# Kernel optimization log

Hardware: AMD Instinct MI355X
Metric: run time of the kernel (lower is better)

The kernel has to match this reference:

```python
import jax, jax.numpy as jnp
import numpy as np

B, R, L, K = 64, 196, 512, 768
NEG = jnp.float32(-2**31 + 1)


def setup_inputs() -> dict:
    key = jax.random.key(0)
    ks = jax.random.split(key, 8)
    image_emb = jax.random.normal(ks[0], (B, R, L), dtype=jnp.float32)
    seq_emb = jax.random.normal(ks[1], (B, L, K), dtype=jnp.float32)
    mask = jax.random.randint(ks[2], (B, L), 0, 2, dtype=jnp.int32)
    # Linear(l,1) and Linear(k,1) params, Xavier-ish scale
    image_W = jax.random.normal(ks[3], (L, 1), dtype=jnp.float32) / np.sqrt(L)
    image_b = jnp.zeros((1,), dtype=jnp.float32)
    seq_W = jax.random.normal(ks[4], (K, 1), dtype=jnp.float32) / np.sqrt(K)
    seq_b = jnp.zeros((1,), dtype=jnp.float32)
    # V_weight [L, L], xavier_uniform
    lim = np.sqrt(6.0 / (L + L)).astype(np.float32)
    V_weight = jax.random.uniform(ks[5], (L, L), dtype=jnp.float32, minval=-lim, maxval=lim)
    return {"image_emb": image_emb, "seq_emb": seq_emb, "mask": mask,
            "image_W": image_W, "image_b": image_b,
            "seq_W": seq_W, "seq_b": seq_b, "V_weight": V_weight}


def reference(image_emb, seq_emb, mask, image_W, image_b, seq_W, seq_b, V_weight):
    # p: [B,R,1], q: [B,L,1]
    p = jnp.tanh(image_emb @ image_W + image_b)
    q = jnp.tanh(seq_emb @ seq_W + seq_b)
    qt = jnp.swapaxes(q, 1, 2)              # [B,1,L]
    emb = p @ qt + qt                       # [B,R,L] (rank-1 outer + broadcast add)
    score = emb @ V_weight                  # [B,R,L]
    # dropout_rate=0.0 -> identity
    score = jnp.where(mask[:, None, :] == 0, NEG, score)
    score = jax.nn.softmax(score, axis=-1)  # [B,R,L]
    out = score @ seq_emb                   # [B,R,K]
    out = out / jnp.sqrt(jnp.float32(seq_emb.shape[-1]))
    return out
```

## Files before the change

kernel.cpp:

```cpp
#include <hip/hip_runtime.h>
#include <cstdint>
#include <cstddef>


typedef __attribute__((ext_vector_type(8))) short short8;
typedef __attribute__((ext_vector_type(4))) float f32x4;

__device__ __forceinline__ unsigned short f32_to_bf16(float x) {
    unsigned int u = __float_as_uint(x);
    unsigned int r = (u + 0x7FFFu + ((u >> 16) & 1u)) >> 16;
    return (unsigned short)r;
}
__device__ __forceinline__ float bf16_to_f32(unsigned short h) {
    return __uint_as_float(((unsigned int)h) << 16);
}

#if defined(__has_builtin)
#if __has_builtin(__builtin_amdgcn_cvt_pk_bf16_f32)
#define HAVE_PK_BF16 1
#endif
#endif

__device__ __forceinline__ unsigned int pk_bf16(float a, float b) {
#ifdef HAVE_PK_BF16
    typedef __attribute__((ext_vector_type(2))) __bf16 bf16x2;
    bf16x2 v = __builtin_amdgcn_cvt_pk_bf16_f32(a, b);
    return __builtin_bit_cast(unsigned int, v);
#else
    return (unsigned int)f32_to_bf16(a) | ((unsigned int)f32_to_bf16(b) << 16);
#endif
}

__global__ __launch_bounds__(256) void kprep(const float* __restrict__ seq,
                                             const float* __restrict__ seqW,
                                             const float* __restrict__ img,
                                             const float* __restrict__ imgW,
                                             const float* __restrict__ imgBias,
                                             unsigned short* __restrict__ seqT,
                                             float* __restrict__ qpart,
                                             float* __restrict__ pv) {
    __shared__ __align__(16) unsigned int sT[128 * 32];
    __shared__ __align__(16) float sWc[128];

    if (blockIdx.x >= 3072) {
        int wv = threadIdx.x >> 6, lane = threadIdx.x & 63;
        int row = (blockIdx.x - 3072) * 4 + wv;
        const float4* x4 = (const float4*)(img + (size_t)row * 512);
        const float4* w4 = (const float4*)imgW;
        float s = 0.f;
#pragma unroll
        for (int i = 0; i < 2; ++i) {
            float4 a = x4[i * 64 + lane];
            float4 c = w4[i * 64 + lane];
            s += a.x * c.x + a.y * c.y + a.z * c.z + a.w * c.w;
        }
#pragma unroll
        for (int o = 32; o; o >>= 1) s += __shfl_xor(s, o, 64);
        if (lane == 0) pv[row] = tanhf(s + imgBias[0]);
        return;
    }

    int id = blockIdx.x;
    int b = id / 48, rem = id - b * 48;
    int jt = rem / 6, ck = rem - jt * 6;
    int j0 = jt * 64;
    int t = threadIdx.x;
    if (t < 128) sWc[t] = seqW[ck * 128 + t];

    int quad = t >> 4, kseg = t & 15;
    int qk = quad ^ kseg;
    const float* base = seq + (size_t)b * 512 * 768 + (size_t)(j0 + quad * 4) * 768 + ck * 128;
    int jg = t & 7, krow = t >> 3;
    float qp[4] = {0.f, 0.f, 0.f, 0.f};
    __syncthreads();

#pragma unroll
    for (int rp = 0; rp < 2; ++rp) {
        int kq = rp * 64 + kseg * 4;
        float4 r0 = *(const float4*)(base + 0 * 768 + kq);
        float4 r1 = *(const float4*)(base + 1 * 768 + kq);
        float4 r2 = *(const float4*)(base + 2 * 768 + kq);
        float4 r3 = *(const float4*)(base + 3 * 768 + kq);
        float4 w  = *(const float4*)(sWc + kq);
        qp[0] += r0.x * w.x + r0.y * w.y + r0.z * w.z + r0.w * w.w;
        qp[1] += r1.x * w.x + r1.y * w.y + r1.z * w.z + r1.w * w.w;
        qp[2] += r2.x * w.x + r2.y * w.y + r2.z * w.z + r2.w * w.w;
        qp[3] += r3.x * w.x + r3.y * w.y + r3.z * w.z + r3.w * w.w;
        float a0[4] = {r0.x, r0.y, r0.z, r0.w};
        float a1[4] = {r1.x, r1.y, r1.z, r1.w};
        float a2[4] = {r2.x, r2.y, r2.z, r2.w};
        float a3[4] = {r3.x, r3.y, r3.z, r3.w};
#pragma unroll
        for (int i = 0; i < 4; ++i) {
            int k = kq + i;
            int col = (qk ^ (i << 2)) & 15;
            uint2 v;
            v.x = pk_bf16(a0[i], a1[i]);
            v.y = pk_bf16(a2[i], a3[i]);
            *(uint2*)(sT + k * 32 + col * 2) = v;
        }
    }
    __syncthreads();
    unsigned short* dst = seqT + (((size_t)b * 6 + ck) * 8 + jt) * (128 * 64);
#pragma unroll
    for (int wp = 0; wp < 4; ++wp) {
        int k = wp * 32 + krow;
        int s = ((k >> 2) & 15) ^ ((k & 3) << 2);
        int sw = (k ^ (k >> 3)) & 7;
        int jgOut = jg ^ sw;
        int c0 = ((jgOut << 1) ^ s) & 15;
        int c1 = c0 ^ 1;
        uint2 va = *(const uint2*)(sT + k * 32 + c0 * 2);
        uint2 vb = *(const uint2*)(sT + k * 32 + c1 * 2);
        uint4 o;
        o.x = va.x; o.y = va.y; o.z = vb.x; o.w = vb.y;
        *(uint4*)(dst + (size_t)k * 64 + jg * 8) = o;
    }
#pragma unroll
    for (int rr = 0; rr < 4; ++rr) {
        float s = qp[rr];
        s += __shfl_xor(s, 8, 64);
        s += __shfl_xor(s, 4, 64);
        s += __shfl_xor(s, 2, 64);
        s += __shfl_xor(s, 1, 64);
        if (kseg == 0)
            qpart[(size_t)ck * 32768 + b * 512 + j0 + quad * 4 + rr] = s;
    }
}

__global__ __launch_bounds__(256) void krows_p(const float* __restrict__ x,
                                               const float* __restrict__ w,
                                               const float* __restrict__ bias,
                                               float* __restrict__ outp) {
    int wv = threadIdx.x >> 6, lane = threadIdx.x & 63;
    int row = blockIdx.x * 4 + wv;
    const float4* x4 = (const float4*)(x + (size_t)row * 512);
    const float4* w4 = (const float4*)w;
    float s = 0.f;
#pragma unroll
    for (int i = 0; i < 2; ++i) {
        float4 a = x4[i * 64 + lane];
        float4 c = w4[i * 64 + lane];
        s += a.x * c.x + a.y * c.y + a.z * c.z + a.w * c.w;
    }
#pragma unroll
    for (int o = 32; o; o >>= 1) s += __shfl_xor(s, o, 64);
    if (lane == 0) outp[row] = tanhf(s + bias[0]);
}

__global__ __launch_bounds__(256) void krows_q(const float* __restrict__ x,
                                               const float* __restrict__ w,
                                               float* __restrict__ outp) {
    int wv = threadIdx.x >> 6, lane = threadIdx.x & 63;
    int row = blockIdx.x * 4 + wv;
    const float4* x4 = (const float4*)(x + (size_t)row * 768);
    const float4* w4 = (const float4*)w;
    float s = 0.f;
#pragma unroll
    for (int i = 0; i < 3; ++i) {
        float4 a = x4[i * 64 + lane];
        float4 c = w4[i * 64 + lane];
        s += a.x * c.x + a.y * c.y + a.z * c.z + a.w * c.w;
    }
#pragma unroll
    for (int o = 32; o; o >>= 1) s += __shfl_xor(s, o, 64);
    if (lane == 0) outp[row] = s;
}

__global__ __launch_bounds__(256) void kw(const float* __restrict__ qpart,
                                          const float* __restrict__ seqBias,
                                          const float* __restrict__ V,
                                          const int* __restrict__ mask,
                                          float* __restrict__ wm,
                                          int nparts) {
    __shared__ __align__(16) float sq[512];
    __shared__ __align__(16) float sacc[16][16][4];
    int b = blockIdx.x >> 3, jc = blockIdx.x & 7;
    int t = threadIdx.x;
    float qb = seqBias[0];
    float a0 = 0.f, a1 = 0.f;
    for (int pp = 0; pp < nparts; ++pp) {
        a0 += qpart[(size_t)pp * 32768 + b * 512 + t];
        a1 += qpart[(size_t)pp * 32768 + b * 512 + t + 256];
    }
    sq[t] = tanhf(a0 + qb);
    sq[t + 256] = tanhf(a1 + qb);
    __syncthreads();
    int jt = t & 15, lg = t >> 4;
    const float4* V4 = (const float4*)V;
    int col4 = jc * 16 + jt;
    float ax = 0.f, ay = 0.f, az = 0.f, aw = 0.f;
    int lbase = lg * 32;
#pragma unroll 8
    for (int li = 0; li < 32; ++li) {
        int l = lbase + li;
        float qq = sq[l];
        float4 v = V4[(size_t)l * 128 + col4];
        ax += qq * v.x; ay += qq * v.y; az += qq * v.z; aw += qq * v.w;
    }
    sacc[lg][jt][0] = ax; sacc[lg][jt][1] = ay;
    sacc[lg][jt][2] = az; sacc[lg][jt][3] = aw;
    __syncthreads();
    if (t < 16) {
        float sx = 0.f, sy = 0.f, sz = 0.f, sw = 0.f;
#pragma unroll
        for (int g = 0; g < 16; ++g) {
            sx += sacc[g][t][0]; sy += sacc[g][t][1];
            sz += sacc[g][t][2]; sw += sacc[g][t][3];
        }
        const int* mrow = mask + b * 512 + jc * 64 + t * 4;
        float4 o;
        o.x = mrow[0] ? sx : -1e30f;
        o.y = mrow[1] ? sy : -1e30f;
        o.z = mrow[2] ? sz : -1e30f;
        o.w = mrow[3] ? sw : -1e30f;
        ((float4*)(wm + b * 512 + jc * 64))[t] = o;
    }
}

__global__ __launch_bounds__(256, 2) void kattn2(const unsigned short* __restrict__ seqT,
                                                 const float* __restrict__ p,
                                                 const float* __restrict__ wm,
                                                 float* __restrict__ out) {
    __shared__ __align__(16) unsigned short sB[2][128 * 64];
    __shared__ __align__(16) float swm[512];
    __shared__ float sinvz[64];
    __shared__ float sred[16];

    int raw = blockIdx.x;
    int g  = ((raw >> 5) << 3) + (raw & 7);
    int rt = (raw >> 3) & 3;
    int b  = g / 6, nt = g - b * 6;
    int t  = threadIdx.x;
    int wv = t >> 6, lane = t & 63;
    int mm = lane & 15, q = lane >> 4;
    int nb = nt * 128;

    float v0 = wm[b * 512 + t];
    float v1 = wm[b * 512 + t + 256];
    swm[t] = v0; swm[t + 256] = v1;
    float lmax = fmaxf(v0, v1);
    float fa = (v0 > -1e29f) ? v0 : 1e30f;
    float fb = (v1 > -1e29f) ? v1 : 1e30f;
    float lmin = fminf(fa, fb);
#pragma unroll
    for (int o = 32; o; o >>= 1) {
        lmax = fmaxf(lmax, __shfl_xor(lmax, o, 64));
        lmin = fminf(lmin, __shfl_xor(lmin, o, 64));
    }
    if (lane == 0) { sred[wv] = lmax; sred[8 + wv] = lmin; }
    __syncthreads();

    bool wactive = (rt * 64 + wv * 16) < 196;

    int rl = wv * 16 + mm;
    int r  = rt * 64 + rl;
    bool valid = r < 196;

    short8 afrag[16];
    if (wactive) {
        float wmax = fmaxf(fmaxf(sred[0], sred[1]), fmaxf(sred[2], sred[3]));
        float wmin = fminf(fminf(sred[8], sred[9]), fminf(sred[10], sred[11]));
        int pidx = b * 196 + (valid ? r : 195);
        float c = 1.0f + p[pidx];
        float M = (c >= 0.f) ? c * wmax : c * wmin;

        float zsum = 0.f;
        const f32x4* swm4 = (const f32x4*)swm;
#pragma unroll
        for (int tk = 0; tk < 16; ++tk) {
            int jb = tk * 32 + q * 8;
            f32x4 w0 = swm4[jb >> 2];
            f32x4 w1 = swm4[(jb >> 2) + 1];
            short8 af;
#pragma unroll
            for (int jj = 0; jj < 8; ++jj) {
                float ww = (jj < 4) ? w0[jj] : w1[jj - 4];
                float e = valid ? __expf(c * ww - M) : 0.f;
                unsigned short h = f32_to_bf16(e);
                zsum += bf16_to_f32(h);
                af[jj] = (short)h;
            }
            afrag[tk] = af;
        }
        zsum += __shfl_xor(zsum, 16, 64);
        zsum += __shfl_xor(zsum, 32, 64);
        if (q == 0) sinvz[rl] = 1.0f / zsum;
    }

    f32x4 acc[8];
#pragma unroll
    for (int s = 0; s < 8; ++s) acc[s] = (f32x4){0.f, 0.f, 0.f, 0.f};

    const unsigned short* seqTb = seqT + ((size_t)(b * 6 + nt) * 8) * (128 * 64);
    int toff = t * 8;
    auto stage = [&](int ch, int buf) {
        const unsigned short* src = seqTb + (size_t)ch * 8192 + toff;
        unsigned short* ld = sB[buf] + toff;
        short8 v0 = *(const short8*)(src);
        short8 v1 = *(const short8*)(src + 2048);
        short8 v2 = *(const short8*)(src + 4096);
        short8 v3 = *(const short8*)(src + 6144);
        *(short8*)(ld)        = v0;
        *(short8*)(ld + 2048) = v1;
        *(short8*)(ld + 4096) = v2;
        *(short8*)(ld + 6144) = v3;
    };

    __syncthreads();
    stage(0, 0);
    __syncthreads();
#pragma unroll
    for (int ch = 0; ch < 8; ++ch) {
        if (ch < 7) stage(ch + 1, (ch + 1) & 1);
        if (wactive) {
            const unsigned short* cb = sB[ch & 1];
#pragma unroll
            for (int kk = 0; kk < 2; ++kk) {
                short8 bfr[8];
#pragma unroll
                for (int s = 0; s < 8; ++s) {
                    int n = s * 16 + mm;
                    int sw = (n ^ (n >> 3)) & 7;
                    bfr[s] = *(const short8*)(cb + n * 64 + ((((kk << 2) + q) ^ sw) << 3));
                }
#pragma unroll
                for (int s = 0; s < 8; ++s)
                    acc[s] = __builtin_amdgcn_mfma_f32_16x16x32_bf16(
                        afrag[(ch << 1) + kk], bfr[s], acc[s], 0, 0, 0);
            }
        }
        __syncthreads();
    }

    if (wactive) {
        const float invsqrtk = 0.036084391824351615f;
#pragma unroll
        for (int reg = 0; reg < 4; ++reg) {
            int row = q * 4 + reg;
            int rr = rt * 64 + wv * 16 + row;
            if (rr < 196) {
                float scale = sinvz[wv * 16 + row] * invsqrtk;
                float* op = out + (size_t)(b * 196 + rr) * 768 + nb + mm;
#pragma unroll
                for (int s = 0; s < 8; ++s)
                    op[s * 16] = acc[s][reg] * scale;
            }
        }
    }
}

__global__ __launch_bounds__(256, 2) void kattn(const float* __restrict__ seq,
                                                const float* __restrict__ p,
                                                const float* __restrict__ wm,
                                                float* __restrict__ out) {
    __shared__ __align__(16) unsigned int sseq[2][128 * 32];
    __shared__ __align__(16) float swm[512];
    __shared__ float sinvz[64];
    __shared__ float sred[16];

    int id = blockIdx.x;
    int rt = id & 3;
    int nt = (id >> 2) % 6;
    int b  = id / 24;
    int t  = threadIdx.x;
    int wv = t >> 6, lane = t & 63;
    int mm = lane & 15, q = lane >> 4;
    int nb = nt * 128;

    float v0 = wm[b * 512 + t];
    float v1 = wm[b * 512 + t + 256];
    swm[t] = v0; swm[t + 256] = v1;
    float lmax = fmaxf(v0, v1);
    float fa = (v0 > -1e29f) ? v0 : 1e30f;
    float fb = (v1 > -1e29f) ? v1 : 1e30f;
    float lmin = fminf(fa, fb);
#pragma unroll
    for (int o = 32; o; o >>= 1) {
        lmax = fmaxf(lmax, __shfl_xor(lmax, o, 64));
        lmin = fminf(lmin, __shfl_xor(lmin, o, 64));
    }
    if (lane == 0) { sred[wv] = lmax; sred[8 + wv] = lmin; }
    __syncthreads();
    float wmax = fmaxf(fmaxf(sred[0], sred[1]), fmaxf(sred[2], sred[3]));
    float wmin = fminf(fminf(sred[8], sred[9]), fminf(sred[10], sred[11]));

    int rl = wv * 16 + mm;
    int r  = rt * 64 + rl;
    bool valid = r < 196;
    int pidx = b * 196 + (valid ? r : 195);
    float c = 1.0f + p[pidx];
    float M = (c >= 0.f) ? c * wmax : c * wmin;

    short8 afrag[16];
    float zsum = 0.f;
    const f32x4* swm4 = (const f32x4*)swm;
#pragma unroll
    for (int tk = 0; tk < 16; ++tk) {
        int jb = tk * 32 + q * 8;
        f32x4 w0 = swm4[jb >> 2];
        f32x4 w1 = swm4[(jb >> 2) + 1];
        short8 af;
#pragma unroll
        for (int jj = 0; jj < 8; ++jj) {
            float ww = (jj < 4) ? w0[jj] : w1[jj - 4];
            float e = valid ? __expf(c * ww - M) : 0.f;
            unsigned short h = f32_to_bf16(e);
            zsum += bf16_to_f32(h);
            af[jj] = (short)h;
        }
        afrag[tk] = af;
    }
    zsum += __shfl_xor(zsum, 16, 64);
    zsum += __shfl_xor(zsum, 32, 64);
    if (q == 0) sinvz[rl] = 1.0f / zsum;

    f32x4 acc[8];
#pragma unroll
    for (int s = 0; s < 8; ++s) acc[s] = (f32x4){0.f, 0.f, 0.f, 0.f};

    const float* seqb = seq + (size_t)b * 512 * 768 + nb;
    int tl = t & 31, jp = t >> 5;
    int n0 = tl * 4;
    auto stage = [&](int ch, int buf) {
        unsigned int* sb = sseq[buf];
#pragma unroll
        for (int pass = 0; pass < 4; ++pass) {
            int jl = pass * 16 + jp * 2;
            int jglob = ch * 64 + jl;
            float4 a0 = *(const float4*)(seqb + (size_t)jglob * 768 + n0);
            float4 a1 = *(const float4*)(seqb + (size_t)(jglob + 1) * 768 + n0);
            float a0v[4] = {a0.x, a0.y, a0.z, a0.w};
            float a1v[4] = {a1.x, a1.y, a1.z, a1.w};
            int g = jl >> 3;
            int wo = (jl & 7) >> 1;
#pragma unroll
            for (int i = 0; i < 4; ++i) {
                int n = n0 + i;
                int sw = (n ^ (n >> 3)) & 7;
                unsigned int pk = (unsigned int)f32_to_bf16(a0v[i]) |
                                  ((unsigned int)f32_to_bf16(a1v[i]) << 16);
                sb[n * 32 + ((g ^ sw) << 2) + wo] = pk;
            }
        }
    };

    __syncthreads();
    stage(0, 0);
    __syncthreads();
#pragma unroll
    for (int ch = 0; ch < 8; ++ch) {
        if (ch < 7) stage(ch + 1, (ch + 1) & 1);
        const unsigned int* cb = sseq[ch & 1];
#pragma unroll
        for (int kk = 0; kk < 2; ++kk) {
            short8 bfr[8];
#pragma unroll
            for (int s = 0; s < 8; ++s) {
                int n = s * 16 + mm;
                int g = kk * 4 + q;
                int sw = (n ^ (n >> 3)) & 7;
                bfr[s] = *(const short8*)(cb + n * 32 + ((g ^ sw) << 2));
            }
#pragma unroll
            for (int s = 0; s < 8; ++s)
                acc[s] = __builtin_amdgcn_mfma_f32_16x16x32_bf16(
                    afrag[ch * 2 + kk], bfr[s], acc[s], 0, 0, 0);
        }
        __syncthreads();
    }

    const float invsqrtk = 0.036084391824351615f;
#pragma unroll
    for (int reg = 0; reg < 4; ++reg) {
        int row = q * 4 + reg;
        int rr = rt * 64 + wv * 16 + row;
        if (rr < 196) {
            float scale = sinvz[wv * 16 + row] * invsqrtk;
            float* op = out + (size_t)(b * 196 + rr) * 768 + nb + mm;
#pragma unroll
            for (int s = 0; s < 8; ++s)
                op[s * 16] = acc[s][reg] * scale;
        }
    }
}

extern "C" void kernel_launch(void* const* d_in, const int* in_sizes, int n_in,
                              void* d_out, int out_size, void* d_ws, size_t ws_size,
                              hipStream_t stream) {
    const float* image_emb = (const float*)d_in[0];
    const float* seq_emb   = (const float*)d_in[1];
    const int*   mask      = (const int*)d_in[2];
    const float* image_W   = (const float*)d_in[3];
    const float* image_b   = (const float*)d_in[4];
    const float* seq_W     = (const float*)d_in[5];
    const float* seq_b     = (const float*)d_in[6];
    const float* V         = (const float*)d_in[7];
    float* out = (float*)d_out;

    float* p_ws  = (float*)d_ws;
    float* qpart = (float*)((char*)d_ws + (128 << 10));
    float* wm_ws = (float*)((char*)d_ws + (896 << 10));
    unsigned short* seqT = (unsigned short*)((char*)d_ws + (1024 << 10));

    size_t need = (size_t)(1024 << 10) + (size_t)64 * 768 * 512 * 2;
    if (ws_size >= need) {
        kprep<<<dim3(6208), dim3(256), 0, stream>>>(seq_emb, seq_W,
                                                    image_emb, image_W, image_b,
                                                    seqT, qpart, p_ws);
        kw<<<dim3(512), dim3(256), 0, stream>>>(qpart, seq_b, V, mask, wm_ws, 6);
        kattn2<<<dim3(1536), dim3(256), 0, stream>>>(seqT, p_ws, wm_ws, out);
    } else {
        krows_p<<<dim3(3136), dim3(256), 0, stream>>>(image_emb, image_W, image_b, p_ws);
        krows_q<<<dim3(8192), dim3(256), 0, stream>>>(seq_emb, seq_W, qpart);
        kw<<<dim3(512), dim3(256), 0, stream>>>(qpart, seq_b, V, mask, wm_ws, 1);
        kattn<<<dim3(1536), dim3(256), 0, stream>>>(seq_emb, p_ws, wm_ws, out);
    }
}
```

Measured before the change: 234.0 us.

## Drop bf16 transposed seq copy; stream fp32 seq directly with register-prefetch pipeline

Removes the prep pass that wrote a transposed bf16 copy of seq_emb to workspace. The attention kernel now reads fp32 seq_emb directly. Loads for the next chunk are issued into registers before the MFMA work and written to shared memory afterward, so global latency overlaps compute. Also merges the q and p row-dot kernels into one launch and skips inactive waves. This saves a full write and re-read of a 50MB intermediate, at the cost of reading fp32 (twice the bytes) inside attention and converting it per block across 6 column tiles.

New measurement: 252.7 us. +8.0%, slower.

```diff
diff --git a/kernel.cpp b/kernel.cpp
--- a/kernel.cpp
+++ b/kernel.cpp
@@ -31,20 +31,30 @@
 #endif
 }
 
-__global__ __launch_bounds__(256) void kprep(const float* __restrict__ seq,
-                                             const float* __restrict__ seqW,
-                                             const float* __restrict__ img,
-                                             const float* __restrict__ imgW,
-                                             const float* __restrict__ imgBias,
-                                             unsigned short* __restrict__ seqT,
-                                             float* __restrict__ qpart,
-                                             float* __restrict__ pv) {
-    __shared__ __align__(16) unsigned int sT[128 * 32];
-    __shared__ __align__(16) float sWc[128];
-
-    if (blockIdx.x >= 3072) {
-        int wv = threadIdx.x >> 6, lane = threadIdx.x & 63;
-        int row = (blockIdx.x - 3072) * 4 + wv;
+__global__ __launch_bounds__(256) void kqp(const float* __restrict__ seq,
+                                           const float* __restrict__ seqW,
+                                           const float* __restrict__ img,
+                                           const float* __restrict__ imgW,
+                                           const float* __restrict__ imgBias,
+                                           float* __restrict__ qraw,
+                                           float* __restrict__ pv) {
+    int wv = threadIdx.x >> 6, lane = threadIdx.x & 63;
+    if (blockIdx.x < 8192) {
+        int row = blockIdx.x * 4 + wv;
+        const float4* x4 = (const float4*)(seq + (size_t)row * 768);
+        const float4* w4 = (const float4*)seqW;
+        float s = 0.f;
+#pragma unroll
+        for (int i = 0; i < 3; ++i) {
+            float4 a = x4[i * 64 + lane];
+            float4 c = w4[i * 64 + lane];
+            s += a.x * c.x + a.y * c.y + a.z * c.z + a.w * c.w;
+        }
+#pragma unroll
+        for (int o = 32; o; o >>= 1) s += __shfl_xor(s, o, 64);
+        if (lane == 0) qraw[row] = s;
+    } else {
+        int row = (blockIdx.x - 8192) * 4 + wv;
         const float4* x4 = (const float4*)(img + (size_t)row * 512);
         const float4* w4 = (const float4*)imgW;
         float s = 0.f;
@@ -57,134 +67,21 @@
 #pragma unroll
         for (int o = 32; o; o >>= 1) s += __shfl_xor(s, o, 64);
         if (lane == 0) pv[row] = tanhf(s + imgBias[0]);
-        return;
-    }
-
-    int id = blockIdx.x;
-    int b = id / 48, rem = id - b * 48;
-    int jt = rem / 6, ck = rem - jt * 6;
-    int j0 = jt * 64;
-    int t = threadIdx.x;
-    if (t < 128) sWc[t] = seqW[ck * 128 + t];
-
-    int quad = t >> 4, kseg = t & 15;
-    int qk = quad ^ kseg;
-    const float* base = seq + (size_t)b * 512 * 768 + (size_t)(j0 + quad * 4) * 768 + ck * 128;
-    int jg = t & 7, krow = t >> 3;
-    float qp[4] = {0.f, 0.f, 0.f, 0.f};
-    __syncthreads();
-
-#pragma unroll
-    for (int rp = 0; rp < 2; ++rp) {
-        int kq = rp * 64 + kseg * 4;
-        float4 r0 = *(const float4*)(base + 0 * 768 + kq);
-        float4 r1 = *(const float4*)(base + 1 * 768 + kq);
-        float4 r2 = *(const float4*)(base + 2 * 768 + kq);
-        float4 r3 = *(const float4*)(base + 3 * 768 + kq);
-        float4 w  = *(const float4*)(sWc + kq);
-        qp[0] += r0.x * w.x + r0.y * w.y + r0.z * w.z + r0.w * w.w;
-        qp[1] += r1.x * w.x + r1.y * w.y + r1.z * w.z + r1.w * w.w;
-        qp[2] += r2.x * w.x + r2.y * w.y + r2.z * w.z + r2.w * w.w;
-        qp[3] += r3.x * w.x + r3.y * w.y + r3.z * w.z + r3.w * w.w;
-        float a0[4] = {r0.x, r0.y, r0.z, r0.w};
-        float a1[4] = {r1.x, r1.y, r1.z, r1.w};
-        float a2[4] = {r2.x, r2.y, r2.z, r2.w};
-        float a3[4] = {r3.x, r3.y, r3.z, r3.w};
-#pragma unroll
-        for (int i = 0; i < 4; ++i) {
-            int k = kq + i;
-            int col = (qk ^ (i << 2)) & 15;
-            uint2 v;
-            v.x = pk_bf16(a0[i], a1[i]);
-            v.y = pk_bf16(a2[i], a3[i]);
-            *(uint2*)(sT + k * 32 + col * 2) = v;
-        }
-    }
-    __syncthreads();
-    unsigned short* dst = seqT + (((size_t)b * 6 + ck) * 8 + jt) * (128 * 64);
-#pragma unroll
-    for (int wp = 0; wp < 4; ++wp) {
-        int k = wp * 32 + krow;
-        int s = ((k >> 2) & 15) ^ ((k & 3) << 2);
-        int sw = (k ^ (k >> 3)) & 7;
-        int jgOut = jg ^ sw;
-        int c0 = ((jgOut << 1) ^ s) & 15;
-        int c1 = c0 ^ 1;
-        uint2 va = *(const uint2*)(sT + k * 32 + c0 * 2);
-        uint2 vb = *(const uint2*)(sT + k * 32 + c1 * 2);
-        uint4 o;
-        o.x = va.x; o.y = va.y; o.z = vb.x; o.w = vb.y;
-        *(uint4*)(dst + (size_t)k * 64 + jg * 8) = o;
-    }
-#pragma unroll
-    for (int rr = 0; rr < 4; ++rr) {
-        float s = qp[rr];
-        s += __shfl_xor(s, 8, 64);
-        s += __shfl_xor(s, 4, 64);
-        s += __shfl_xor(s, 2, 64);
-        s += __shfl_xor(s, 1, 64);
-        if (kseg == 0)
-            qpart[(size_t)ck * 32768 + b * 512 + j0 + quad * 4 + rr] = s;
-    }
-}
-
-__global__ __launch_bounds__(256) void krows_p(const float* __restrict__ x,
-                                               const float* __restrict__ w,
-                                               const float* __restrict__ bias,
-                                               float* __restrict__ outp) {
-    int wv = threadIdx.x >> 6, lane = threadIdx.x & 63;
-    int row = blockIdx.x * 4 + wv;
-    const float4* x4 = (const float4*)(x + (size_t)row * 512);
-    const float4* w4 = (const float4*)w;
-    float s = 0.f;
-#pragma unroll
-    for (int i = 0; i < 2; ++i) {
-        float4 a = x4[i * 64 + lane];
-        float4 c = w4[i * 64 + lane];
-        s += a.x * c.x + a.y * c.y + a.z * c.z + a.w * c.w;
-    }
-#pragma unroll
-    for (int o = 32; o; o >>= 1) s += __shfl_xor(s, o, 64);
-    if (lane == 0) outp[row] = tanhf(s + bias[0]);
-}
-
-__global__ __launch_bounds__(256) void krows_q(const float* __restrict__ x,
-                                               const float* __restrict__ w,
-                                               float* __restrict__ outp) {
-    int wv = threadIdx.x >> 6, lane = threadIdx.x & 63;
-    int row = blockIdx.x * 4 + wv;
-    const float4* x4 = (const float4*)(x + (size_t)row * 768);
-    const float4* w4 = (const float4*)w;
-    float s = 0.f;
-#pragma unroll
-    for (int i = 0; i < 3; ++i) {
-        float4 a = x4[i * 64 + lane];
-        float4 c = w4[i * 64 + lane];
-        s += a.x * c.x + a.y * c.y + a.z * c.z + a.w * c.w;
-    }
-#pragma unroll
-    for (int o = 32; o; o >>= 1) s += __shfl_xor(s, o, 64);
-    if (lane == 0) outp[row] = s;
-}
-
-__global__ __launch_bounds__(256) void kw(const float* __restrict__ qpart,
+    }
+}
+
+__global__ __launch_bounds__(256) void kw(const float* __restrict__ qraw,
                                           const float* __restrict__ seqBias,
                                           const float* __restrict__ V,
                                           const int* __restrict__ mask,
-                                          float* __restrict__ wm,
-                                          int nparts) {
+                                          float* __restrict__ wm) {
     __shared__ __align__(16) float sq[512];
     __shared__ __align__(16) float sacc[16][16][4];
     int b = blockIdx.x >> 3, jc = blockIdx.x & 7;
     int t = threadIdx.x;
     float qb = seqBias[0];
-    float a0 = 0.f, a1 = 0.f;
-    for (int pp = 0; pp < nparts; ++pp) {
-        a0 += qpart[(size_t)pp * 32768 + b * 512 + t];
-        a1 += qpart[(size_t)pp * 32768 + b * 512 + t + 256];
-    }
-    sq[t] = tanhf(a0 + qb);
-    sq[t + 256] = tanhf(a1 + qb);
+    sq[t] = tanhf(qraw[b * 512 + t] + qb);
+    sq[t + 256] = tanhf(qraw[b * 512 + t + 256] + qb);
     __syncthreads();
     int jt = t & 15, lg = t >> 4;
     const float4* V4 = (const float4*)V;
@@ -218,138 +115,6 @@
     }
 }
 
-__global__ __launch_bounds__(256, 2) void kattn2(const unsigned short* __restrict__ seqT,
-                                                 const float* __restrict__ p,
-                                                 const float* __restrict__ wm,
-                                                 float* __restrict__ out) {
-    __shared__ __align__(16) unsigned short sB[2][128 * 64];
-    __shared__ __align__(16) float swm[512];
-    __shared__ float sinvz[64];
-    __shared__ float sred[16];
-
-    int raw = blockIdx.x;
-    int g  = ((raw >> 5) << 3) + (raw & 7);
-    int rt = (raw >> 3) & 3;
-    int b  = g / 6, nt = g - b * 6;
-    int t  = threadIdx.x;
-    int wv = t >> 6, lane = t & 63;
-    int mm = lane & 15, q = lane >> 4;
-    int nb = nt * 128;
-
-    float v0 = wm[b * 512 + t];
-    float v1 = wm[b * 512 + t + 256];
-    swm[t] = v0; swm[t + 256] = v1;
-    float lmax = fmaxf(v0, v1);
-    float fa = (v0 > -1e29f) ? v0 : 1e30f;
-    float fb = (v1 > -1e29f) ? v1 : 1e30f;
-    float lmin = fminf(fa, fb);
-#pragma unroll
-    for (int o = 32; o; o >>= 1) {
-        lmax = fmaxf(lmax, __shfl_xor(lmax, o, 64));
-        lmin = fminf(lmin, __shfl_xor(lmin, o, 64));
-    }
-    if (lane == 0) { sred[wv] = lmax; sred[8 + wv] = lmin; }
-    __syncthreads();
-
-    bool wactive = (rt * 64 + wv * 16) < 196;
-
-    int rl = wv * 16 + mm;
-    int r  = rt * 64 + rl;
-    bool valid = r < 196;
-
-    short8 afrag[16];
-    if (wactive) {
-        float wmax = fmaxf(fmaxf(sred[0], sred[1]), fmaxf(sred[2], sred[3]));
-        float wmin = fminf(fminf(sred[8], sred[9]), fminf(sred[10], sred[11]));
-        int pidx = b * 196 + (valid ? r : 195);
-        float c = 1.0f + p[pidx];
-        float M = (c >= 0.f) ? c * wmax : c * wmin;
-
-        float zsum = 0.f;
-        const f32x4* swm4 = (const f32x4*)swm;
-#pragma unroll
-        for (int tk = 0; tk < 16; ++tk) {
-            int jb = tk * 32 + q * 8;
-            f32x4 w0 = swm4[jb >> 2];
-            f32x4 w1 = swm4[(jb >> 2) + 1];
-            short8 af;
-#pragma unroll
-            for (int jj = 0; jj < 8; ++jj) {
-                float ww = (jj < 4) ? w0[jj] : w1[jj - 4];
-                float e = valid ? __expf(c * ww - M) : 0.f;
-                unsigned short h = f32_to_bf16(e);
-                zsum += bf16_to_f32(h);
-                af[jj] = (short)h;
-            }
-            afrag[tk] = af;
-        }
-        zsum += __shfl_xor(zsum, 16, 64);
-        zsum += __shfl_xor(zsum, 32, 64);
-        if (q == 0) sinvz[rl] = 1.0f / zsum;
-    }
-
-    f32x4 acc[8];
-#pragma unroll
-    for (int s = 0; s < 8; ++s) acc[s] = (f32x4){0.f, 0.f, 0.f, 0.f};
-
-    const unsigned short* seqTb = seqT + ((size_t)(b * 6 + nt) * 8) * (128 * 64);
-    int toff = t * 8;
-    auto stage = [&](int ch, int buf) {
-        const unsigned short* src = seqTb + (size_t)ch * 8192 + toff;
-        unsigned short* ld = sB[buf] + toff;
-        short8 v0 = *(const short8*)(src);
-        short8 v1 = *(const short8*)(src + 2048);
-        short8 v2 = *(const short8*)(src + 4096);
-        short8 v3 = *(const short8*)(src + 6144);
-        *(short8*)(ld)        = v0;
-        *(short8*)(ld + 2048) = v1;
-        *(short8*)(ld + 4096) = v2;
-        *(short8*)(ld + 6144) = v3;
-    };
-
-    __syncthreads();
-    stage(0, 0);
-    __syncthreads();
-#pragma unroll
-    for (int ch = 0; ch < 8; ++ch) {
-        if (ch < 7) stage(ch + 1, (ch + 1) & 1);
-        if (wactive) {
-            const unsigned short* cb = sB[ch & 1];
-#pragma unroll
-            for (int kk = 0; kk < 2; ++kk) {
-                short8 bfr[8];
-#pragma unroll
-                for (int s = 0; s < 8; ++s) {
-                    int n = s * 16 + mm;
-                    int sw = (n ^ (n >> 3)) & 7;
-                    bfr[s] = *(const short8*)(cb + n * 64 + ((((kk << 2) + q) ^ sw) << 3));
-                }
-#pragma unroll
-                for (int s = 0; s < 8; ++s)
-                    acc[s] = __builtin_amdgcn_mfma_f32_16x16x32_bf16(
-                        afrag[(ch << 1) + kk], bfr[s], acc[s], 0, 0, 0);
-            }
-        }
-        __syncthreads();
-    }
-
-    if (wactive) {
-        const float invsqrtk = 0.036084391824351615f;
-#pragma unroll
-        for (int reg = 0; reg < 4; ++reg) {
-            int row = q * 4 + reg;
-            int rr = rt * 64 + wv * 16 + row;
-            if (rr < 196) {
-                float scale = sinvz[wv * 16 + row] * invsqrtk;
-                float* op = out + (size_t)(b * 196 + rr) * 768 + nb + mm;
-#pragma unroll
-                for (int s = 0; s < 8; ++s)
-                    op[s * 16] = acc[s][reg] * scale;
-            }
-        }
-    }
-}
-
 __global__ __launch_bounds__(256, 2) void kattn(const float* __restrict__ seq,
                                                 const float* __restrict__ p,
                                                 const float* __restrict__ wm,
@@ -368,6 +133,40 @@
     int mm = lane & 15, q = lane >> 4;
     int nb = nt * 128;
 
+    const float* seqb = seq + (size_t)b * 512 * 768 + nb;
+    int tl = t & 31, jp = t >> 5;
+    int n0 = tl * 4;
+
+    float4 A0[4], A1[4];
+    auto stage_load = [&](int ch) {
+#pragma unroll
+        for (int pass = 0; pass < 4; ++pass) {
+            int jl = pass * 16 + jp * 2;
+            int jglob = ch * 64 + jl;
+            A0[pass] = *(const float4*)(seqb + (size_t)jglob * 768 + n0);
+            A1[pass] = *(const float4*)(seqb + (size_t)(jglob + 1) * 768 + n0);
+        }
+    };
+    auto stage_write = [&](int buf) {
+        unsigned int* sb = sseq[buf];
+#pragma unroll
+        for (int pass = 0; pass < 4; ++pass) {
+            int jl = pass * 16 + jp * 2;
+            int g = jl >> 3;
+            int wo = (jl & 7) >> 1;
+            float a0v[4] = {A0[pass].x, A0[pass].y, A0[pass].z, A0[pass].w};
+            float a1v[4] = {A1[pass].x, A1[pass].y, A1[pass].z, A1[pass].w};
+#pragma unroll
+            for (int i = 0; i < 4; ++i) {
+                int n = n0 + i;
+                int sw = (n ^ (n >> 3)) & 7;
+                sb[n * 32 + ((g ^ sw) << 2) + wo] = pk_bf16(a0v[i], a1v[i]);
+            }
+        }
+    };
+
+    stage_load(0);
+
     float v0 = wm[b * 512 + t];
     float v1 = wm[b * 512 + t + 256];
     swm[t] = v0; swm[t + 256] = v1;
@@ -382,105 +181,87 @@
     }
     if (lane == 0) { sred[wv] = lmax; sred[8 + wv] = lmin; }
     __syncthreads();
-    float wmax = fmaxf(fmaxf(sred[0], sred[1]), fmaxf(sred[2], sred[3]));
-    float wmin = fminf(fminf(sred[8], sred[9]), fminf(sred[10], sred[11]));
-
+
+    bool wactive = (rt * 64 + wv * 16) < 196;
     int rl = wv * 16 + mm;
     int r  = rt * 64 + rl;
     bool valid = r < 196;
-    int pidx = b * 196 + (valid ? r : 195);
-    float c = 1.0f + p[pidx];
-    float M = (c >= 0.f) ? c * wmax : c * wmin;
 
     short8 afrag[16];
-    float zsum = 0.f;
-    const f32x4* swm4 = (const f32x4*)swm;
-#pragma unroll
-    for (int tk = 0; tk < 16; ++tk) {
-        int jb = tk * 32 + q * 8;
-        f32x4 w0 = swm4[jb >> 2];
-        f32x4 w1 = swm4[(jb >> 2) + 1];
-        short8 af;
-#pragma unroll
-        for (int jj = 0; jj < 8; ++jj) {
-            float ww = (jj < 4) ? w0[jj] : w1[jj - 4];
-            float e = valid ? __expf(c * ww - M) : 0.f;
-            unsigned short h = f32_to_bf16(e);
-            zsum += bf16_to_f32(h);
-            af[jj] = (short)h;
-        }
-        afrag[tk] = af;
-    }
-    zsum += __shfl_xor(zsum, 16, 64);
-    zsum += __shfl_xor(zsum, 32, 64);
-    if (q == 0) sinvz[rl] = 1.0f / zsum;
+    if (wactive) {
+        float wmax = fmaxf(fmaxf(sred[0], sred[1]), fmaxf(sred[2], sred[3]));
+        float wmin = fminf(fminf(sred[8], sred[9]), fminf(sred[10], sred[11]));
+        int pidx = b * 196 + (valid ? r : 195);
+        float c = 1.0f + p[pidx];
+        float M = (c >= 0.f) ? c * wmax : c * wmin;
+
+        float zsum = 0.f;
+        const f32x4* swm4 = (const f32x4*)swm;
+#pragma unroll
+        for (int tk = 0; tk < 16; ++tk) {
+            int jb = tk * 32 + q * 8;
+            f32x4 w0 = swm4[jb >> 2];
+            f32x4 w1 = swm4[(jb >> 2) + 1];
+            short8 af;
+#pragma unroll
+            for (int jj = 0; jj < 8; ++jj) {
+                float ww = (jj < 4) ? w0[jj] : w1[jj - 4];
+                float e = valid ? __expf(c * ww - M) : 0.f;
+                unsigned short h = f32_to_bf16(e);
+                zsum += bf16_to_f32(h);
+                af[jj] = (short)h;
+            }
+            afrag[tk] = af;
+        }
+        zsum += __shfl_xor(zsum, 16, 64);
+        zsum += __shfl_xor(zsum, 32, 64);
+        if (q == 0) sinvz[rl] = 1.0f / zsum;
+    }
 
     f32x4 acc[8];
 #pragma unroll
     for (int s = 0; s < 8; ++s) acc[s] = (f32x4){0.f, 0.f, 0.f, 0.f};
 
-    const float* seqb = seq + (size_t)b * 512 * 768 + nb;
-    int tl = t & 31, jp = t >> 5;
-    int n0 = tl * 4;
-    auto stage = [&](int ch, int buf) {
-        unsigned int* sb = sseq[buf];
-#pragma unroll
-        for (int pass = 0; pass < 4; ++pass) {
-            int jl = pass * 16 + jp * 2;
-            int jglob = ch * 64 + jl;
-            float4 a0 = *(const float4*)(seqb + (size_t)jglob * 768 + n0);
-            float4 a1 = *(const float4*)(seqb + (size_t)(jglob + 1) * 768 + n0);
-            float a0v[4] = {a0.x, a0.y, a0.z, a0.w};
-            float a1v[4] = {a1.x, a1.y, a1.z, a1.w};
-            int g = jl >> 3;
-            int wo = (jl & 7) >> 1;
-#pragma unroll
-            for (int i = 0; i < 4; ++i) {
-                int n = n0 + i;
-                int sw = (n ^ (n >> 3)) & 7;
-                unsigned int pk = (unsigned int)f32_to_bf16(a0v[i]) |
-                                  ((unsigned int)f32_to_bf16(a1v[i]) << 16);
-                sb[n * 32 + ((g ^ sw) << 2) + wo] = pk;
-            }
-        }
-    };
-
-    __syncthreads();
-    stage(0, 0);
+    stage_write(0);
     __syncthreads();
 #pragma unroll
     for (int ch = 0; ch < 8; ++ch) {
-        if (ch < 7) stage(ch + 1, (ch + 1) & 1);
-        const unsigned int* cb = sseq[ch & 1];
-#pragma unroll
-        for (int kk = 0; kk < 2; ++kk) {
-            short8 bfr[8];
-#pragma unroll
-            for (int s = 0; s < 8; ++s) {
-                int n = s * 16 + mm;
-                int g = kk * 4 + q;
-                int sw = (n ^ (n >> 3)) & 7;
-                bfr[s] = *(const short8*)(cb + n * 32 + ((g ^ sw) << 2));
-            }
-#pragma unroll
-            for (int s = 0; s < 8; ++s)
-                acc[s] = __builtin_amdgcn_mfma_f32_16x16x32_bf16(
-                    afrag[ch * 2 + kk], bfr[s], acc[s], 0, 0, 0);
-        }
+        if (ch < 7) stage_load(ch + 1);
+        if (wactive) {
+            const unsigned int* cb = sseq[ch & 1];
+#pragma unroll
+            for (int kk = 0; kk < 2; ++kk) {
+                short8 bfr[8];
+#pragma unroll
+                for (int s = 0; s < 8; ++s) {
+                    int n = s * 16 + mm;
+                    int g = kk * 4 + q;
+                    int sw = (n ^ (n >> 3)) & 7;
+                    bfr[s] = *(const short8*)(cb + n * 32 + ((g ^ sw) << 2));
+                }
+#pragma unroll
+                for (int s = 0; s < 8; ++s)
+                    acc[s] = __builtin_amdgcn_mfma_f32_16x16x32_bf16(
+                        afrag[ch * 2 + kk], bfr[s], acc[s], 0, 0, 0);
+            }
+        }
+        if (ch < 7) stage_write((ch + 1) & 1);
         __syncthreads();
     }
 
-    const float invsqrtk = 0.036084391824351615f;
-#pragma unroll
-    for (int reg = 0; reg < 4; ++reg) {
-        int row = q * 4 + reg;
-        int rr = rt * 64 + wv * 16 + row;
-        if (rr < 196) {
-            float scale = sinvz[wv * 16 + row] * invsqrtk;
-            float* op = out + (size_t)(b * 196 + rr) * 768 + nb + mm;
-#pragma unroll
-            for (int s = 0; s < 8; ++s)
-                op[s * 16] = acc[s][reg] * scale;
+    if (wactive) {
+        const float invsqrtk = 0.036084391824351615f;
+#pragma unroll
+        for (int reg = 0; reg < 4; ++reg) {
+            int row = q * 4 + reg;
+            int rr = rt * 64 + wv * 16 + row;
+            if (rr < 196) {
+                float scale = sinvz[wv * 16 + row] * invsqrtk;
+                float* op = out + (size_t)(b * 196 + rr) * 768 + nb + mm;
+#pragma unroll
+                for (int s = 0; s < 8; ++s)
+                    op[s * 16] = acc[s][reg] * scale;
+            }
         }
     }
 }
@@ -498,22 +279,13 @@
     const float* V         = (const float*)d_in[7];
     float* out = (float*)d_out;
 
-    float* p_ws  = (float*)d_ws;
-    float* qpart = (float*)((char*)d_ws + (128 << 10));
-    float* wm_ws = (float*)((char*)d_ws + (896 << 10));
-    unsigned short* seqT = (unsigned short*)((char*)d_ws + (1024 << 10));
-
-    size_t need = (size_t)(1024 << 10) + (size_t)64 * 768 * 512 * 2;
-    if (ws_size >= need) {
-        kprep<<<dim3(6208), dim3(256), 0, stream>>>(seq_emb, seq_W,
-                                                    image_emb, image_W, image_b,
-                                                    seqT, qpart, p_ws);
-        kw<<<dim3(512), dim3(256), 0, stream>>>(qpart, seq_b, V, mask, wm_ws, 6);
-        kattn2<<<dim3(1536), dim3(256), 0, stream>>>(seqT, p_ws, wm_ws, out);
-    } else {
-        krows_p<<<dim3(3136), dim3(256), 0, stream>>>(image_emb, image_W, image_b, p_ws);
-        krows_q<<<dim3(8192), dim3(256), 0, stream>>>(seq_emb, seq_W, qpart);
-        kw<<<dim3(512), dim3(256), 0, stream>>>(qpart, seq_b, V, mask, wm_ws, 1);
-        kattn<<<dim3(1536), dim3(256), 0, stream>>>(seq_emb, p_ws, wm_ws, out);
-    }
-}
+    float* p_ws = (float*)d_ws;
+    float* q_ws = (float*)((char*)d_ws + (128 << 10));
+    float* wm_ws = (float*)((char*)d_ws + (256 << 10));
+
+    kqp<<<dim3(11328), dim3(256), 0, stream>>>(seq_emb, seq_W,
+                                               image_emb, image_W, image_b,
+                                               q_ws, p_ws);
+    kw<<<dim3(512), dim3(256), 0, stream>>>(q_ws, seq_b, V, mask, wm_ws);
+    kattn<<<dim3(1536), dim3(256), 0, stream>>>(seq_emb, p_ws, wm_ws, out);
+}
```
